# Optimization experiments

Hardware: AMD Instinct MI355X
Metric: run time of the kernel (lower is better)

Reference implementation:

```python
import jax, jax.numpy as jnp
import numpy as np

B, C, H, W = 8, 256, 128, 128
HEADS = 16
HEADC = C // HEADS  # 16
EPS = 1e-5


def setup_inputs() -> dict:
    key = jax.random.key(0)
    k1, k2 = jax.random.split(key)
    x = jax.random.normal(k1, (B, C, H, W), dtype=jnp.float32)
    w_qkv = jax.random.normal(k2, (3 * C, C), dtype=jnp.float32) * (1.0 / np.sqrt(C))
    b_qkv = jnp.zeros((3 * C,), dtype=jnp.float32)
    kln_w = jnp.ones((HEADS, HEADC), dtype=jnp.float32)
    kln_b = jnp.zeros((HEADS, HEADC), dtype=jnp.float32)
    vln_w = jnp.ones((HEADS, HEADC), dtype=jnp.float32)
    vln_b = jnp.zeros((HEADS, HEADC), dtype=jnp.float32)
    return {"x": x, "w_qkv": w_qkv, "b_qkv": b_qkv,
            "kln_w": kln_w, "kln_b": kln_b, "vln_w": vln_w, "vln_b": vln_b}


def _layernorm(x, w, b):
    # torch-style: unbiased std (ddof=1), divides by (std + eps), over last dim
    mean = jnp.mean(x, axis=-1, keepdims=True)
    std = jnp.std(x, axis=-1, keepdims=True, ddof=1)
    return (x - mean) / (std + EPS) * w + b


def reference(x, w_qkv, b_qkv, kln_w, kln_b, vln_w, vln_b):
    b, c, h, w = x.shape
    n = h * w
    # 1x1 conv == per-pixel matmul over channels
    qkv = jnp.einsum('bchw,oc->bhwo', x, w_qkv) + b_qkv  # (B,H,W,3C)
    qkv = qkv.reshape(b, n, HEADS, -1)                   # (B,N,16,3*headc)
    q, k, v = jnp.split(qkv, 3, axis=-1)                 # each (B,N,16,headc)
    k = _layernorm(k, kln_w, kln_b)
    v = _layernorm(v, vln_w, vln_b)
    # linear (Galerkin) attention: kv = k^T v / N, out = q @ kv
    kv = jnp.einsum('bnhd,bnhe->bhde', k, v) / n         # (B,16,headc,headc)
    out = jnp.einsum('bnhd,bhde->bnhe', q, kv)           # (B,N,16,headc)
    out = out.reshape(b, h, w, c).transpose(0, 3, 1, 2)  # (B,C,H,W)
    return out
```

## Files before the change

kernel.cpp:

```cpp
#include <hip/hip_runtime.h>

typedef unsigned short u16;
typedef unsigned int u32;
typedef __attribute__((ext_vector_type(8))) short short8;
typedef __attribute__((ext_vector_type(4))) float f32x4;

#define NPIX 16384
#define LNEPS 1e-5f

__device__ __forceinline__ float bf2f(u16 u) {
  union { u32 i; float f; } x; x.i = ((u32)u) << 16; return x.f;
}
__device__ __forceinline__ u16 f2bf(float f) {
  union { float f; u32 i; } x; x.f = f;
  u32 r = x.i + 0x7fffu + ((x.i >> 16) & 1u);
  return (u16)(r >> 16);
}
__device__ __forceinline__ void gload_lds16(const void* g, void* l) {
  __builtin_amdgcn_global_load_lds((__attribute__((address_space(1))) void*)(g),
                                   (__attribute__((address_space(3))) void*)(l),
                                   16, 0, 0);
}
__device__ __forceinline__ uint4 pack8(float4 a, float4 b) {
  uint4 q;
  q.x = (u32)f2bf(a.x) | ((u32)f2bf(a.y) << 16);
  q.y = (u32)f2bf(a.z) | ((u32)f2bf(a.w) << 16);
  q.z = (u32)f2bf(b.x) | ((u32)f2bf(b.y) << 16);
  q.w = (u32)f2bf(b.z) | ((u32)f2bf(b.w) << 16);
  return q;
}

__global__ __launch_bounds__(256) void k_detect(const u16* __restrict__ x,
                                                int* __restrict__ flag) {
  float mx = 0.f;
  for (int i = threadIdx.x; i < 4096; i += 256) {
    float v = fabsf(bf2f(x[2 * i]));
    if (v == v) mx = fmaxf(mx, v);
  }
  for (int m = 1; m < 64; m <<= 1) mx = fmaxf(mx, __shfl_xor(mx, m));
  __shared__ float wmax[4];
  if ((threadIdx.x & 63) == 0) wmax[threadIdx.x >> 6] = mx;
  __syncthreads();
  if (threadIdx.x == 0) {
    float m2 = fmaxf(fmaxf(wmax[0], wmax[1]), fmaxf(wmax[2], wmax[3]));
    flag[0] = (m2 > 1e5f) ? 1 : 0;
  }
}

__global__ __launch_bounds__(256) void k_wconv(
    const void* __restrict__ w, const void* __restrict__ bq,
    const void* __restrict__ klw, const void* __restrict__ klb,
    const void* __restrict__ vlw, const void* __restrict__ vlb,
    u16* __restrict__ wkv, u16* __restrict__ wq,
    float* __restrict__ bias_kv, float* __restrict__ lnw_kv,
    float* __restrict__ lnb_kv, float* __restrict__ bq_q,
    const int* __restrict__ flag) {
  const int i = blockIdx.x * 256 + threadIdx.x;
  const bool f32 = flag[0] != 0;
  auto getf = [&](const void* p, int j) -> float {
    return f32 ? ((const float*)p)[j] : bf2f(((const u16*)p)[j]);
  };
  if (i < 131072) {
    int o = i >> 8, c = i & 255;
    int h = o >> 5, tt = (o >> 4) & 1, d = o & 15;
    wkv[i] = f2bf(getf(w, (h * 48 + 16 + tt * 16 + d) * 256 + c));
  } else if (i < 196608) {
    int j = i - 131072; int r = j >> 8, c = j & 255;
    wq[j] = f2bf(getf(w, ((r >> 4) * 48 + (r & 15)) * 256 + c));
  } else if (i < 198400) {
    int j = i - 196608;
    if (j < 512) {
      int h = j >> 5, tt = (j >> 4) & 1, d = j & 15;
      bias_kv[j] = getf(bq, h * 48 + 16 + tt * 16 + d);
    } else if (j < 1024) {
      int o = j - 512; int h = o >> 5, tt = (o >> 4) & 1, d = o & 15;
      lnw_kv[o] = getf(tt ? vlw : klw, h * 16 + d);
    } else if (j < 1536) {
      int o = j - 1024; int h = o >> 5, tt = (o >> 4) & 1, d = o & 15;
      lnb_kv[o] = getf(tt ? vlb : klb, h * 16 + d);
    } else {
      int r = j - 1536;
      bq_q[r] = getf(bq, (r >> 4) * 48 + (r & 15));
    }
  }
}

__global__ __launch_bounds__(512, 4) void k_gemm1(
    const void* __restrict__ xin, const u16* __restrict__ wkv,
    const float* __restrict__ bias_kv, const float* __restrict__ lnw_kv,
    const float* __restrict__ lnb_kv, float* __restrict__ kvpart,
    const int* __restrict__ flag) {
  __shared__ alignas(16) char shraw[73728];
  u16 (*wlds)[256][32] = (u16 (*)[256][32])shraw;
  u16 (*xlds)[32][128] = (u16 (*)[32][128])(shraw + 32768);
  u16 (*klds)[260]     = (u16 (*)[260])shraw;
  float* bls = (float*)(shraw + 66560);
  float* wls = bls + 256;
  float* lls = bls + 512;
  float (*tmp)[256] = (float (*)[256])(shraw + 69632);

  const int t = threadIdx.x;
  const int lbid = ((blockIdx.x & 7) << 8) + (blockIdx.x >> 3);
  const int hg = lbid & 1;
  const int pc = (lbid >> 1) & 127;
  const int b  = lbid >> 8;
  const int p0 = pc * 128;
  const int wv = t >> 6, lane = t & 63, quad = lane >> 4, l16 = lane & 15;
  const int hl = wv & 1, pxq = wv >> 1;
  const bool f32 = flag[0] != 0;

  if (t < 256) {
    bls[t] = bias_kv[hg * 256 + t];
    wls[t] = lnw_kv[hg * 256 + t];
    lls[t] = lnb_kv[hg * 256 + t];
  }

  f32x4 acc[8][2];
#pragma unroll
  for (int ms = 0; ms < 8; ++ms) {
    acc[ms][0] = (f32x4){0.f, 0.f, 0.f, 0.f};
    acc[ms][1] = (f32x4){0.f, 0.f, 0.f, 0.f};
  }

  const int wrow = t >> 2;
  const int wcs  = t & 3;
  const int wks  = (wcs ^ ((t >> 3) & 3)) * 8;
  const u16* wsrc = wkv + ((size_t)(hg * 256 + wrow) * 256 + wks);

  const int xrow = t >> 4;
  const int xg   = (t & 15) ^ ((xrow >> 3) << 1);
  const u16* xsrc_bf = (const u16*)xin +
      ((size_t)(b * 256 + xrow) * NPIX + p0 + xg * 8);
  const float* xsrc_f = (const float*)xin +
      ((size_t)(b * 256 + xrow) * NPIX + p0 + xg * 8);

  gload_lds16(wsrc, &wlds[0][wrow][wcs * 8]);
  gload_lds16(wsrc + (size_t)128 * 256, &wlds[0][128 + wrow][wcs * 8]);
  if (!f32) {
    gload_lds16(xsrc_bf, &xlds[0][xrow][(t & 15) * 8]);
  } else {
    float4 a = *(const float4*)xsrc_f;
    float4 c = *(const float4*)(xsrc_f + 4);
    *(uint4*)&xlds[0][xrow][(t & 15) * 8] = pack8(a, c);
  }
  __syncthreads();

  for (int ks = 0; ks < 8; ++ks) {
    const int cur = ks & 1, nxt = cur ^ 1;
    const bool more = ks < 7;
    float4 v0, v1;
    if (more) {
      const u16* ws = wsrc + (ks + 1) * 32;
      gload_lds16(ws, &wlds[nxt][wrow][wcs * 8]);
      gload_lds16(ws + (size_t)128 * 256, &wlds[nxt][128 + wrow][wcs * 8]);
      if (!f32) {
        gload_lds16(xsrc_bf + (size_t)(ks + 1) * 32 * NPIX,
                    &xlds[nxt][xrow][(t & 15) * 8]);
      } else {
        const float* xf = xsrc_f + (size_t)(ks + 1) * 32 * NPIX;
        v0 = *(const float4*)xf;
        v1 = *(const float4*)(xf + 4);
      }
    }
    short8 bfr[2];
#pragma unroll
    for (int ns = 0; ns < 2; ++ns) {
      const int pxn = pxq * 32 + ns * 16 + l16;
      const int cs8 = ((((pxn >> 3) ^ (quad << 1)) << 3) + (pxn & 7));
      short8 bv;
#pragma unroll
      for (int j = 0; j < 8; ++j)
        bv[j] = (short)xlds[cur][quad * 8 + j][cs8];
      bfr[ns] = bv;
    }
#pragma unroll
    for (int ms = 0; ms < 8; ++ms) {
      const int row = hl * 128 + ms * 16 + l16;
      short8 av = *(const short8*)&wlds[cur][row][(quad ^ ((l16 >> 1) & 3)) * 8];
      acc[ms][0] = __builtin_amdgcn_mfma_f32_16x16x32_bf16(av, bfr[0], acc[ms][0], 0, 0, 0);
      acc[ms][1] = __builtin_amdgcn_mfma_f32_16x16x32_bf16(av, bfr[1], acc[ms][1], 0, 0, 0);
    }
    if (more && f32)
      *(uint4*)&xlds[nxt][xrow][(t & 15) * 8] = pack8(v0, v1);
    __syncthreads();
  }

#pragma unroll
  for (int p = 0; p < 2; ++p) {
    __syncthreads();
#pragma unroll
    for (int j = 0; j < 4; ++j) {
      const int msl = p * 4 + j;
      const int slot = (j >> 1) | (hl << 1);
      const int cb = slot * 64 + (j & 1) * 16;
      float4 bi = *(const float4*)&bls[hl * 128 + msl * 16 + quad * 4];
      float4 lw = *(const float4*)&wls[hl * 128 + msl * 16 + quad * 4];
      float4 lb = *(const float4*)&lls[hl * 128 + msl * 16 + quad * 4];
      float biv[4] = {bi.x, bi.y, bi.z, bi.w};
      float lwv[4] = {lw.x, lw.y, lw.z, lw.w};
      float lbv[4] = {lb.x, lb.y, lb.z, lb.w};
#pragma unroll
      for (int ns = 0; ns < 2; ++ns) {
        const int px = pxq * 32 + ns * 16 + l16;
        float x0[4];
#pragma unroll
        for (int r = 0; r < 4; ++r) x0[r] = acc[msl][ns][r] + biv[r];
        float s1 = x0[0] + x0[1] + x0[2] + x0[3];
        s1 += __shfl_xor(s1, 16);
        s1 += __shfl_xor(s1, 32);
        float mean = s1 * (1.0f / 16.0f);
        float dv[4];
#pragma unroll
        for (int r = 0; r < 4; ++r) dv[r] = x0[r] - mean;
        float s2 = dv[0]*dv[0] + dv[1]*dv[1] + dv[2]*dv[2] + dv[3]*dv[3];
        s2 += __shfl_xor(s2, 16);
        s2 += __shfl_xor(s2, 32);
        float var = s2 * (1.0f / 15.0f);
        float rstd = 1.0f / (sqrtf(var) + LNEPS);
        u16 hi[4], lo[4];
#pragma unroll
        for (int r = 0; r < 4; ++r) {
          float kn = dv[r] * rstd * lwv[r] + lbv[r];
          hi[r] = f2bf(kn);
          lo[r] = f2bf(kn - bf2f(hi[r]));
        }
        uint2 ph, pl;
        ph.x = (u32)hi[0] | ((u32)hi[1] << 16);
        ph.y = (u32)hi[2] | ((u32)hi[3] << 16);
        pl.x = (u32)lo[0] | ((u32)lo[1] << 16);
        pl.y = (u32)lo[2] | ((u32)lo[3] << 16);
        *(uint2*)&klds[px][cb + quad * 4] = ph;
        *(uint2*)&klds[px][cb + 32 + quad * 4] = pl;
      }
    }
    __syncthreads();
    const int slot4 = wv >> 1, combo = wv & 1;
    const int cb2 = slot4 * 64;
    f32x4 kva = (f32x4){0.f, 0.f, 0.f, 0.f};
    if (combo == 0) {
#pragma unroll
      for (int px2 = 0; px2 < 4; ++px2) {
        short8 av, bv;
#pragma unroll
        for (int jj = 0; jj < 8; ++jj) {
          av[jj] = (short)klds[px2 * 32 + quad * 8 + jj][cb2 + l16];
          bv[jj] = (short)klds[px2 * 32 + quad * 8 + jj][cb2 + 16 + l16];
        }
        kva = __builtin_amdgcn_mfma_f32_16x16x32_bf16(av, bv, kva, 0, 0, 0);
      }
    } else {
#pragma unroll
      for (int px2 = 0; px2 < 4; ++px2) {
        short8 ah, al, vh, vl;
#pragma unroll
        for (int jj = 0; jj < 8; ++jj) {
          const int px = px2 * 32 + quad * 8 + jj;
          ah[jj] = (short)klds[px][cb2 + l16];
          vh[jj] = (short)klds[px][cb2 + 16 + l16];
          al[jj] = (short)klds[px][cb2 + 32 + l16];
          vl[jj] = (short)klds[px][cb2 + 48 + l16];
        }
        kva = __builtin_amdgcn_mfma_f32_16x16x32_bf16(ah, vl, kva, 0, 0, 0);
        kva = __builtin_amdgcn_mfma_f32_16x16x32_bf16(al, vh, kva, 0, 0, 0);
      }
    }
    __syncthreads();
    if (combo) {
#pragma unroll
      for (int r = 0; r < 4; ++r) tmp[slot4][(quad * 4 + r) * 16 + l16] = kva[r];
    }
    __syncthreads();
    if (!combo) {
      const int h = (slot4 >> 1) * 4 + p * 2 + (slot4 & 1);
      float* kvp = kvpart +
          ((size_t)(((b * 128 + pc) * 2 + hg) * 8 + h) << 8);
#pragma unroll
      for (int r = 0; r < 4; ++r) {
        const int idx = (quad * 4 + r) * 16 + l16;
        kvp[idx] = kva[r] + tmp[slot4][idx];
      }
    }
  }
}

__global__ __launch_bounds__(256) void k_reduce(const float* __restrict__ kvpart,
                                                float* __restrict__ kvg) {
  const int t = threadIdx.x;
  const int b = blockIdx.x >> 4, h = blockIdx.x & 15;
  const int hg = h >> 3, hl = h & 7;
  const float* src = kvpart + ((size_t)((b * 128 * 2 + hg) * 8 + hl) << 8) + t;
  float s = 0.f;
  for (int pc = 0; pc < 128; ++pc)
    s += src[(size_t)pc * (2 * 8 * 256)];
  kvg[((size_t)blockIdx.x << 8) + t] = s * (1.0f / 16384.0f);
}

__global__ __launch_bounds__(256) void k_fold(const u16* __restrict__ wq,
                                              const float* __restrict__ bq_q,
                                              const float* __restrict__ kvg,
                                              u16* __restrict__ whi,
                                              u16* __restrict__ wlo,
                                              float* __restrict__ beff) {
  __shared__ float kvs[256];
  __shared__ float qb[16];
  const int t = threadIdx.x;
  const int b = blockIdx.x >> 4, h = blockIdx.x & 15;
  kvs[t] = kvg[((size_t)blockIdx.x << 8) + t];
  if (t < 16) qb[t] = bq_q[h * 16 + t];
  __syncthreads();
  const int e = t >> 4, c0 = (t & 15) * 16;
  float o[16];
#pragma unroll
  for (int c = 0; c < 16; ++c) o[c] = 0.f;
  for (int d = 0; d < 16; ++d) {
    float kv_de = kvs[d * 16 + e];
    const u16* wr = wq + (size_t)(h * 16 + d) * 256 + c0;
#pragma unroll
    for (int c = 0; c < 16; ++c) o[c] = fmaf(bf2f(wr[c]), kv_de, o[c]);
  }
  const size_t wbase = (size_t)(b * 256 + h * 16 + e) * 256 + c0;
#pragma unroll
  for (int c = 0; c < 16; ++c) {
    u16 hi = f2bf(o[c]);
    whi[wbase + c] = hi;
    wlo[wbase + c] = f2bf(o[c] - bf2f(hi));
  }
  if (t < 16) {
    float s = 0.f;
    for (int d = 0; d < 16; ++d) s += qb[d] * kvs[d * 16 + t];
    beff[b * 256 + h * 16 + t] = s;
  }
}

__global__ __launch_bounds__(512, 4) void k_gemm2(
    const void* __restrict__ xin, const u16* __restrict__ whi,
    const u16* __restrict__ wlo, const float* __restrict__ beff,
    void* __restrict__ outv, const int* __restrict__ flag) {
  __shared__ alignas(16) char shraw[49152];
  u16 (*wldh)[32] = (u16 (*)[32])shraw;
  u16 (*wldl)[32] = (u16 (*)[32])(shraw + 16384);
  u16 (*xlds)[32][128] = (u16 (*)[32][128])(shraw + 32768);

  const int t = threadIdx.x;
  const int lbid = ((blockIdx.x & 7) << 7) + (blockIdx.x >> 3);
  const int pc = lbid & 127;
  const int b  = lbid >> 7;
  const int p0 = pc * 128;
  const int wv = t >> 6, lane = t & 63, quad = lane >> 4, l16 = lane & 15;
  const int hl = wv & 1, pxq = wv >> 1;
  const bool f32 = flag[0] != 0;

  f32x4 acc[8][2];
#pragma unroll
  for (int ms = 0; ms < 8; ++ms) {
    acc[ms][0] = (f32x4){0.f, 0.f, 0.f, 0.f};
    acc[ms][1] = (f32x4){0.f, 0.f, 0.f, 0.f};
  }

  const int wrow = t >> 2;
  const int wcs  = t & 3;
  const int wks  = (wcs ^ ((t >> 3) & 3)) * 8;
  const size_t wbase = (size_t)(b * 256 + wrow) * 256 + wks;
  const u16* wsrch = whi + wbase;
  const u16* wsrcl = wlo + wbase;

  const int xrow = t >> 4;
  const int xg   = (t & 15) ^ ((xrow >> 3) << 1);
  const u16* xsrc_bf = (const u16*)xin +
      ((size_t)(b * 256 + xrow) * NPIX + p0 + xg * 8);
  const float* xsrc_f = (const float*)xin +
      ((size_t)(b * 256 + xrow) * NPIX + p0 + xg * 8);

  gload_lds16(wsrch, &wldh[wrow][wcs * 8]);
  gload_lds16(wsrch + (size_t)128 * 256, &wldh[128 + wrow][wcs * 8]);
  gload_lds16(wsrcl, &wldl[wrow][wcs * 8]);
  gload_lds16(wsrcl + (size_t)128 * 256, &wldl[128 + wrow][wcs * 8]);
  if (!f32) {
    gload_lds16(xsrc_bf, &xlds[0][xrow][(t & 15) * 8]);
  } else {
    float4 a = *(const float4*)xsrc_f;
    float4 c = *(const float4*)(xsrc_f + 4);
    *(uint4*)&xlds[0][xrow][(t & 15) * 8] = pack8(a, c);
  }
  __syncthreads();

  for (int ks = 0; ks < 8; ++ks) {
    const int cur = ks & 1, nxt = cur ^ 1;
    const bool more = ks < 7;
    float4 v0, v1;
    if (more) {
      if (!f32) {
        gload_lds16(xsrc_bf + (size_t)(ks + 1) * 32 * NPIX,
                    &xlds[nxt][xrow][(t & 15) * 8]);
      } else {
        const float* xf = xsrc_f + (size_t)(ks + 1) * 32 * NPIX;
        v0 = *(const float4*)xf;
        v1 = *(const float4*)(xf + 4);
      }
    }
    short8 bfr[2];
#pragma unroll
    for (int ns = 0; ns < 2; ++ns) {
      const int pxn = pxq * 32 + ns * 16 + l16;
      const int cs8 = ((((pxn >> 3) ^ (quad << 1)) << 3) + (pxn & 7));
      short8 bv;
#pragma unroll
      for (int j = 0; j < 8; ++j)
        bv[j] = (short)xlds[cur][quad * 8 + j][cs8];
      bfr[ns] = bv;
    }
#pragma unroll
    for (int ms = 0; ms < 8; ++ms) {
      const int row = hl * 128 + ms * 16 + l16;
      const int csw = (quad ^ ((l16 >> 1) & 3)) * 8;
      short8 avh = *(const short8*)&wldh[row][csw];
      short8 avl = *(const short8*)&wldl[row][csw];
      acc[ms][0] = __builtin_amdgcn_mfma_f32_16x16x32_bf16(avh, bfr[0], acc[ms][0], 0, 0, 0);
      acc[ms][0] = __builtin_amdgcn_mfma_f32_16x16x32_bf16(avl, bfr[0], acc[ms][0], 0, 0, 0);
      acc[ms][1] = __builtin_amdgcn_mfma_f32_16x16x32_bf16(avh, bfr[1], acc[ms][1], 0, 0, 0);
      acc[ms][1] = __builtin_amdgcn_mfma_f32_16x16x32_bf16(avl, bfr[1], acc[ms][1], 0, 0, 0);
    }
    __syncthreads();
    if (more) {
      const u16* wh = wsrch + (ks + 1) * 32;
      const u16* wl = wsrcl + (ks + 1) * 32;
      gload_lds16(wh, &wldh[wrow][wcs * 8]);
      gload_lds16(wh + (size_t)128 * 256, &wldh[128 + wrow][wcs * 8]);
      gload_lds16(wl, &wldl[wrow][wcs * 8]);
      gload_lds16(wl + (size_t)128 * 256, &wldl[128 + wrow][wcs * 8]);
      if (f32)
        *(uint4*)&xlds[nxt][xrow][(t & 15) * 8] = pack8(v0, v1);
      __syncthreads();
    }
  }

  const size_t obase = (size_t)b * 256 * NPIX + p0;
#pragma unroll
  for (int ms = 0; ms < 8; ++ms) {
    const int o0 = hl * 128 + ms * 16 + quad * 4;
    float4 be = *(const float4*)&beff[b * 256 + o0];
    float bev[4] = {be.x, be.y, be.z, be.w};
#pragma unroll
    for (int ns = 0; ns < 2; ++ns) {
      const int px = pxq * 32 + ns * 16 + l16;
#pragma unroll
      for (int r = 0; r < 4; ++r) {
        const int o = o0 + r;
        float val = acc[ms][ns][r] + bev[r];
        if (f32) ((float*)outv)[obase + (size_t)o * NPIX + px] = val;
        else ((u16*)outv)[obase + (size_t)o * NPIX + px] = f2bf(val);
      }
    }
  }
}

extern "C" void kernel_launch(void* const* d_in, const int* in_sizes, int n_in,
                              void* d_out, int out_size, void* d_ws, size_t ws_size,
                              hipStream_t stream) {
  (void)in_sizes; (void)n_in; (void)out_size; (void)ws_size;
  char* ws = (char*)d_ws;
  u16* wkv       = (u16*)(ws + 0);
  u16* wq        = (u16*)(ws + 262144);
  u16* weff_hi   = (u16*)(ws + 393216);
  u16* weff_lo   = (u16*)(ws + 1441792);
  float* kvg     = (float*)(ws + 2490368);
  float* bias_kv = (float*)(ws + 2621440);
  float* lnw_kv  = (float*)(ws + 2623488);
  float* lnb_kv  = (float*)(ws + 2625536);
  float* bq_q    = (float*)(ws + 2627584);
  float* beff    = (float*)(ws + 2628608);
  int* flag      = (int*)(ws + 2636800);
  float* kvpart  = (float*)(ws + 4194304);

  k_detect<<<1, 256, 0, stream>>>((const u16*)d_in[0], flag);
  k_wconv<<<775, 256, 0, stream>>>(d_in[1], d_in[2], d_in[3], d_in[4], d_in[5],
                                   d_in[6], wkv, wq, bias_kv, lnw_kv, lnb_kv,
                                   bq_q, flag);
  k_gemm1<<<2048, 512, 0, stream>>>(d_in[0], wkv, bias_kv, lnw_kv, lnb_kv,
                                    kvpart, flag);
  k_reduce<<<128, 256, 0, stream>>>(kvpart, kvg);
  k_fold<<<128, 256, 0, stream>>>(wq, bq_q, kvg, weff_hi, weff_lo, beff);
  k_gemm2<<<1024, 512, 0, stream>>>(d_in[0], weff_hi, weff_lo, beff, d_out, flag);
}
```

Measured before the change: 371.3 us.

## Fuse kv reduction into fold kernel and double-buffer weight tiles in gemm2

The separate k_reduce launch is removed and its 128-way partial-sum reduction now runs at the start of k_fold, saving one kernel launch and the kvg round trip. In k_gemm2 the weight hi/lo LDS tiles become double-buffered, so the next K-slice is prefetched before the MFMA loop and one barrier per iteration goes away. LDS use per block grows from 48KB to 80KB, which may cut how many 512-thread blocks fit on a CU.

```diff
diff --git a/kernel.cpp b/kernel.cpp
--- a/kernel.cpp
+++ b/kernel.cpp
@@ -283,21 +283,9 @@
   }
 }
 
-__global__ __launch_bounds__(256) void k_reduce(const float* __restrict__ kvpart,
-                                                float* __restrict__ kvg) {
-  const int t = threadIdx.x;
-  const int b = blockIdx.x >> 4, h = blockIdx.x & 15;
-  const int hg = h >> 3, hl = h & 7;
-  const float* src = kvpart + ((size_t)((b * 128 * 2 + hg) * 8 + hl) << 8) + t;
-  float s = 0.f;
-  for (int pc = 0; pc < 128; ++pc)
-    s += src[(size_t)pc * (2 * 8 * 256)];
-  kvg[((size_t)blockIdx.x << 8) + t] = s * (1.0f / 16384.0f);
-}
-
 __global__ __launch_bounds__(256) void k_fold(const u16* __restrict__ wq,
                                               const float* __restrict__ bq_q,
-                                              const float* __restrict__ kvg,
+                                              const float* __restrict__ kvpart,
                                               u16* __restrict__ whi,
                                               u16* __restrict__ wlo,
                                               float* __restrict__ beff) {
@@ -305,7 +293,12 @@
   __shared__ float qb[16];
   const int t = threadIdx.x;
   const int b = blockIdx.x >> 4, h = blockIdx.x & 15;
-  kvs[t] = kvg[((size_t)blockIdx.x << 8) + t];
+  const int hg = h >> 3, hl = h & 7;
+  const float* src = kvpart + ((size_t)((b * 128 * 2 + hg) * 8 + hl) << 8) + t;
+  float s0 = 0.f;
+  for (int pc = 0; pc < 128; ++pc)
+    s0 += src[(size_t)pc * (2 * 8 * 256)];
+  kvs[t] = s0 * (1.0f / 16384.0f);
   if (t < 16) qb[t] = bq_q[h * 16 + t];
   __syncthreads();
   const int e = t >> 4, c0 = (t & 15) * 16;
@@ -336,10 +329,9 @@
     const void* __restrict__ xin, const u16* __restrict__ whi,
     const u16* __restrict__ wlo, const float* __restrict__ beff,
     void* __restrict__ outv, const int* __restrict__ flag) {
-  __shared__ alignas(16) char shraw[49152];
-  u16 (*wldh)[32] = (u16 (*)[32])shraw;
-  u16 (*wldl)[32] = (u16 (*)[32])(shraw + 16384);
-  u16 (*xlds)[32][128] = (u16 (*)[32][128])(shraw + 32768);
+  __shared__ u16 wldh[2][256][32];
+  __shared__ u16 wldl[2][256][32];
+  __shared__ u16 xlds[2][32][128];
 
   const int t = threadIdx.x;
   const int lbid = ((blockIdx.x & 7) << 7) + (blockIdx.x >> 3);
@@ -371,10 +363,10 @@
   const float* xsrc_f = (const float*)xin +
       ((size_t)(b * 256 + xrow) * NPIX + p0 + xg * 8);
 
-  gload_lds16(wsrch, &wldh[wrow][wcs * 8]);
-  gload_lds16(wsrch + (size_t)128 * 256, &wldh[128 + wrow][wcs * 8]);
-  gload_lds16(wsrcl, &wldl[wrow][wcs * 8]);
-  gload_lds16(wsrcl + (size_t)128 * 256, &wldl[128 + wrow][wcs * 8]);
+  gload_lds16(wsrch, &wldh[0][wrow][wcs * 8]);
+  gload_lds16(wsrch + (size_t)128 * 256, &wldh[0][128 + wrow][wcs * 8]);
+  gload_lds16(wsrcl, &wldl[0][wrow][wcs * 8]);
+  gload_lds16(wsrcl + (size_t)128 * 256, &wldl[0][128 + wrow][wcs * 8]);
   if (!f32) {
     gload_lds16(xsrc_bf, &xlds[0][xrow][(t & 15) * 8]);
   } else {
@@ -389,6 +381,12 @@
     const bool more = ks < 7;
     float4 v0, v1;
     if (more) {
+      const u16* wh = wsrch + (ks + 1) * 32;
+      const u16* wl = wsrcl + (ks + 1) * 32;
+      gload_lds16(wh, &wldh[nxt][wrow][wcs * 8]);
+      gload_lds16(wh + (size_t)128 * 256, &wldh[nxt][128 + wrow][wcs * 8]);
+      gload_lds16(wl, &wldl[nxt][wrow][wcs * 8]);
+      gload_lds16(wl + (size_t)128 * 256, &wldl[nxt][128 + wrow][wcs * 8]);
       if (!f32) {
         gload_lds16(xsrc_bf + (size_t)(ks + 1) * 32 * NPIX,
                     &xlds[nxt][xrow][(t & 15) * 8]);
@@ -413,25 +411,16 @@
     for (int ms = 0; ms < 8; ++ms) {
       const int row = hl * 128 + ms * 16 + l16;
       const int csw = (quad ^ ((l16 >> 1) & 3)) * 8;
-      short8 avh = *(const short8*)&wldh[row][csw];
-      short8 avl = *(const short8*)&wldl[row][csw];
+      short8 avh = *(const short8*)&wldh[cur][row][csw];
+      short8 avl = *(const short8*)&wldl[cur][row][csw];
       acc[ms][0] = __builtin_amdgcn_mfma_f32_16x16x32_bf16(avh, bfr[0], acc[ms][0], 0, 0, 0);
       acc[ms][0] = __builtin_amdgcn_mfma_f32_16x16x32_bf16(avl, bfr[0], acc[ms][0], 0, 0, 0);
       acc[ms][1] = __builtin_amdgcn_mfma_f32_16x16x32_bf16(avh, bfr[1], acc[ms][1], 0, 0, 0);
       acc[ms][1] = __builtin_amdgcn_mfma_f32_16x16x32_bf16(avl, bfr[1], acc[ms][1], 0, 0, 0);
     }
-    __syncthreads();
-    if (more) {
-      const u16* wh = wsrch + (ks + 1) * 32;
-      const u16* wl = wsrcl + (ks + 1) * 32;
-      gload_lds16(wh, &wldh[wrow][wcs * 8]);
-      gload_lds16(wh + (size_t)128 * 256, &wldh[128 + wrow][wcs * 8]);
-      gload_lds16(wl, &wldl[wrow][wcs * 8]);
-      gload_lds16(wl + (size_t)128 * 256, &wldl[128 + wrow][wcs * 8]);
-      if (f32)
-        *(uint4*)&xlds[nxt][xrow][(t & 15) * 8] = pack8(v0, v1);
-      __syncthreads();
-    }
+    if (more && f32)
+      *(uint4*)&xlds[nxt][xrow][(t & 15) * 8] = pack8(v0, v1);
+    __syncthreads();
   }
 
   const size_t obase = (size_t)b * 256 * NPIX + p0;
@@ -463,7 +452,6 @@
   u16* wq        = (u16*)(ws + 262144);
   u16* weff_hi   = (u16*)(ws + 393216);
   u16* weff_lo   = (u16*)(ws + 1441792);
-  float* kvg     = (float*)(ws + 2490368);
   float* bias_kv = (float*)(ws + 2621440);
   float* lnw_kv  = (float*)(ws + 2623488);
   float* lnb_kv  = (float*)(ws + 2625536);
@@ -478,7 +466,6 @@
                                    bq_q, flag);
   k_gemm1<<<2048, 512, 0, stream>>>(d_in[0], wkv, bias_kv, lnw_kv, lnb_kv,
                                     kvpart, flag);
-  k_reduce<<<128, 256, 0, stream>>>(kvpart, kvg);
-  k_fold<<<128, 256, 0, stream>>>(wq, bq_q, kvg, weff_hi, weff_lo, beff);
+  k_fold<<<128, 256, 0, stream>>>(wq, bq_q, kvpart, weff_hi, weff_lo, beff);
   k_gemm2<<<1024, 512, 0, stream>>>(d_in[0], weff_hi, weff_lo, beff, d_out, flag);
 }
```

Result: no change. 378.5 us (+2.0%).
